# Kernel tuning notes

Hardware: AMD Instinct MI355X
Metric: run time of the kernel (lower is better)

## Reference

```python
import jax, jax.numpy as jnp
import numpy as np

B, N, H = 64, 512, 512
HC = H // 2  # per-direction GRU hidden


def setup_inputs() -> dict:
    key = jax.random.key(0)
    ks = jax.random.split(key, 10)
    s = 0.05
    return {
        "x": jax.random.normal(ks[0], (B, N, H), jnp.float32),
        "num_nodes": jax.random.randint(ks[1], (B,), 1, N + 1),
        "w_ih": jax.random.normal(ks[2], (2, 2, 3 * HC, H), jnp.float32) * s,
        "w_hh": jax.random.normal(ks[3], (2, 2, 3 * HC, HC), jnp.float32) * s,
        "b_ih": jax.random.normal(ks[4], (2, 2, 3 * HC), jnp.float32) * s,
        "b_hh": jax.random.normal(ks[5], (2, 2, 3 * HC), jnp.float32) * s,
        "ln_gamma": jnp.ones((H,), jnp.float32),
        "ln_beta": jnp.zeros((H,), jnp.float32),
        "w_att": jax.random.normal(ks[6], (2 * H, 1), jnp.float32) * s,
        "attention_query": jax.random.normal(ks[7], (B, H), jnp.float32),
    }


def _gru_dir(x, Wih, Whh, bih, bhh, reverse):
    # x: [B, N, in] -> [B, N, HC]; single-direction GRU via lax.scan
    xg = jnp.einsum('bni,gi->bng', x, Wih) + bih  # precompute input gates [B,N,3HC]
    xs = jnp.swapaxes(xg, 0, 1)  # [N, B, 3HC]

    def step(h, xt):
        hg = jnp.einsum('bh,gh->bg', h, Whh) + bhh
        xr, xz, xn = jnp.split(xt, 3, axis=-1)
        hr, hz, hn = jnp.split(hg, 3, axis=-1)
        r = jax.nn.sigmoid(xr + hr)
        z = jax.nn.sigmoid(xz + hz)
        n = jnp.tanh(xn + r * hn)
        h2 = (1.0 - z) * n + z * h
        return h2, h2

    h0 = jnp.zeros((x.shape[0], HC), x.dtype)
    _, ys = jax.lax.scan(step, h0, xs, reverse=reverse)
    return jnp.swapaxes(ys, 0, 1)  # [B, N, HC]


def _residual_gru(x, w_ih, w_hh, b_ih, b_hh, ln_gamma, ln_beta):
    h = x
    for layer in range(2):
        fwd = _gru_dir(h, w_ih[layer, 0], w_hh[layer, 0], b_ih[layer, 0], b_hh[layer, 0], False)
        bwd = _gru_dir(h, w_ih[layer, 1], w_hh[layer, 1], b_ih[layer, 1], b_hh[layer, 1], True)
        h = jnp.concatenate([fwd, bwd], axis=-1)  # [B, N, H]
    y = h + x  # residual
    mu = jnp.mean(y, axis=-1, keepdims=True)
    var = jnp.mean((y - mu) ** 2, axis=-1, keepdims=True)
    return (y - mu) / jnp.sqrt(var + 1e-5) * ln_gamma + ln_beta


def reference(x, num_nodes, w_ih, w_hh, b_ih, b_hh, ln_gamma, ln_beta, w_att, attention_query):
    # zero-pad past each graph's node count (mirrors the torch pad-to-batch loop)
    mask = (jnp.arange(N)[None, :] < num_nodes[:, None])[:, :, None]
    xp = jnp.where(mask, x, 0.0)
    h = _residual_gru(xp, w_ih, w_hh, b_ih, b_hh, ln_gamma, ln_beta)  # [B, N, H]
    # concat([h, query]) @ w_att == h @ w_att[:H] + q @ w_att[H:]
    scores = jnp.einsum('bnh,ho->bno', h, w_att[:H]) + jnp.einsum('bh,ho->bo', attention_query, w_att[H:])[:, None, :]
    scores = jax.nn.leaky_relu(scores, negative_slope=0.01)
    w = jax.nn.softmax(scores, axis=1)  # [B, N, 1] (unmasked, as original)
    return jnp.sum(h * w, axis=1)  # [B, H]
```

## Files before the change

kernel.cpp:

```cpp
#include <hip/hip_runtime.h>
#include <stdint.h>

typedef __attribute__((ext_vector_type(8))) short short8;
typedef __attribute__((ext_vector_type(4))) float f32x4;

#define DEV static __device__ __forceinline__

#define L2E 1.4426950408889634f

DEV unsigned short f2bf(float f){
  unsigned int u = __float_as_uint(f);
  u = (u + 0x7FFFu + ((u >> 16) & 1u)) >> 16;
  return (unsigned short)u;
}
DEV float bf2f(unsigned short u){
  return __uint_as_float(((unsigned int)u) << 16);
}
DEV float frcp(float x){ return __builtin_amdgcn_rcpf(x); }
DEV float exp2a(float x){ float r; asm("v_exp_f32 %0, %1" : "=v"(r) : "v"(x)); return r; }
DEV float bfu(unsigned int u, int c){
  return c ? __uint_as_float(u & 0xFFFF0000u) : __uint_as_float(u << 16);
}
DEV float wredsum(float v){
  #pragma unroll
  for (int m = 32; m; m >>= 1) v += __shfl_xor(v, m);
  return v;
}
DEV float wredmax(float v){
  #pragma unroll
  for (int m = 32; m; m >>= 1) v = fmaxf(v, __shfl_xor(v, m));
  return v;
}

#define BB 64
#define NN 512
#define HH 512
#define HC 256

__global__ void prep_w(const float* __restrict__ wih, const float* __restrict__ whh,
                       const float* __restrict__ bih, const float* __restrict__ bhh,
                       unsigned short* __restrict__ wihb, unsigned short* __restrict__ whhb,
                       float* __restrict__ cbias)
{
  const int NW1 = 2*2*768*512;
  const int NW2 = 2*2*768*256;
  const int NCB = 2*1536;
  for (int i = blockIdx.x*256 + threadIdx.x; i < NW1+NW2+NCB; i += gridDim.x*256){
    if (i < NW1){
      const int row = (i >> 9) % 768;
      const float sc = ((row >> 8) == 2) ? 2.f*L2E : L2E;
      wihb[i] = f2bf(wih[i] * sc);
    } else if (i < NW1+NW2){
      const int k = i - NW1;
      const int row = (k >> 8) % 768;
      const float sc = ((row >> 8) == 2) ? 2.f*L2E : L2E;
      whhb[k] = f2bf(whh[k] * sc);
    } else {
      int k = i - NW1 - NW2;
      int L = k / 1536, r = k % 1536;
      int dd = r / 768, g = r % 768;
      int idx = (L*2 + dd)*768 + g;
      const float sc = (g >= 512) ? 2.f*L2E : L2E;
      cbias[k] = (bih[idx] + (g < 512 ? bhh[idx] : 0.f)) * sc;
    }
  }
}

__global__ void prep_x(const float* __restrict__ x, const int* __restrict__ nnode,
                       unsigned short* __restrict__ xpb)
{
  const int TOT4 = (BB*NN*HH) >> 2;
  for (int i = blockIdx.x*256 + threadIdx.x; i < TOT4; i += gridDim.x*256){
    const int e = i << 2;
    const int b = e >> 18;
    const int n = (e >> 9) & 511;
    float4 v = *(const float4*)(x + e);
    if (n >= nnode[b]) { v.x = 0.f; v.y = 0.f; v.z = 0.f; v.w = 0.f; }
    ushort4 o;
    o.x = f2bf(v.x); o.y = f2bf(v.y); o.z = f2bf(v.z); o.w = f2bf(v.w);
    *(ushort4*)(xpb + e) = o;
  }
}

__global__ __launch_bounds__(256, 2) void gemm_xg(
    const unsigned short* __restrict__ A,
    const unsigned short* __restrict__ W,
    const float* __restrict__ cbias,
    unsigned short* __restrict__ C)
{
  const int tid = threadIdx.x;
  const int l = tid & 63, wv = tid >> 6;
  const int col = l & 15, lq = l >> 4;
  const int n0 = blockIdx.x * 128;
  const int m0 = blockIdx.y * 128;
  const int wm = wv >> 1, wn = wv & 1;
  __shared__ char As[16384];
  __shared__ char Ws[16384];

  f32x4 acc[4][4];
  #pragma unroll
  for (int a = 0; a < 4; a++)
    #pragma unroll
    for (int b2 = 0; b2 < 4; b2++) acc[a][b2] = (f32x4){0.f,0.f,0.f,0.f};

  short8 pa[4], pw[4];
  #pragma unroll
  for (int p = 0; p < 4; p++){
    const int qq = p*256 + tid, row = qq >> 3, sl = qq & 7;
    pa[p] = *(const short8*)(A + (m0+row)*512 + sl*8);
    pw[p] = *(const short8*)(W + (n0+row)*512 + sl*8);
  }

  for (int ko = 0; ko < 8; ++ko){
    __syncthreads();
    #pragma unroll
    for (int p = 0; p < 4; p++){
      const int qq = p*256 + tid, row = qq >> 3, sl = qq & 7;
      *(short8*)(As + row*128 + ((sl ^ (row & 7)) << 4)) = pa[p];
      *(short8*)(Ws + row*128 + ((sl ^ (row & 7)) << 4)) = pw[p];
    }
    __syncthreads();
    if (ko < 7){
      #pragma unroll
      for (int p = 0; p < 4; p++){
        const int qq = p*256 + tid, row = qq >> 3, sl = qq & 7;
        pa[p] = *(const short8*)(A + (m0+row)*512 + (ko+1)*64 + sl*8);
        pw[p] = *(const short8*)(W + (n0+row)*512 + (ko+1)*64 + sl*8);
      }
    }
    #pragma unroll
    for (int kt = 0; kt < 2; kt++){
      short8 af[4], bfr[4];
      #pragma unroll
      for (int mi = 0; mi < 4; mi++){
        const int r = wm*64 + mi*16 + col;
        af[mi] = *(const short8*)(As + r*128 + ((((kt<<2)|lq) ^ (r & 7)) << 4));
      }
      #pragma unroll
      for (int ni = 0; ni < 4; ni++){
        const int r = wn*64 + ni*16 + col;
        bfr[ni] = *(const short8*)(Ws + r*128 + ((((kt<<2)|lq) ^ (r & 7)) << 4));
      }
      #pragma unroll
      for (int mi = 0; mi < 4; mi++)
        #pragma unroll
        for (int ni = 0; ni < 4; ni++)
          acc[mi][ni] = __builtin_amdgcn_mfma_f32_16x16x32_bf16(af[mi], bfr[ni], acc[mi][ni], 0, 0, 0);
    }
  }
  #pragma unroll
  for (int ni = 0; ni < 4; ni++){
    const int n = n0 + wn*64 + ni*16 + col;
    const int dirn = (n >= 768) ? 1 : 0;
    const int g = n - dirn*768;
    const int cls = g >> 8;
    const int j = g & 255;
    const int noff = dirn*768 + (j >> 5)*96 + (j & 15)*6 + cls*2 + ((j >> 4) & 1);
    const float cb = cbias[n];
    #pragma unroll
    for (int mi = 0; mi < 4; mi++){
      const int m = m0 + wm*64 + mi*16 + lq*4;
      #pragma unroll
      for (int rg = 0; rg < 4; rg++)
        C[(m + rg)*1536 + noff] = f2bf(acc[mi][ni][rg] + cb);
    }
  }
}

#define MFMA16(a,b,c) __builtin_amdgcn_mfma_f32_16x16x32_bf16(a, b, c, 0, 0, 0)

#define GRU_STEP(HB_R, HB_W, PF_CUR, PF_NXT, TCUR, TNEXT) do {                  \
  { const uint3 v3 = *(const uint3*)(xg + xgo + (TNEXT)*1536);                  \
    PF_NXT[0]=v3.x; PF_NXT[1]=v3.y; PF_NXT[2]=v3.z; }                           \
  f32x4 acc0 = (f32x4){0.f,0.f,0.f,0.f};                                        \
  f32x4 acc1 = (f32x4){0.f,0.f,0.f,0.f};                                        \
  f32x4 acc2 = (f32x4){0.f,0.f,0.f,0.f};                                        \
  _Pragma("unroll")                                                             \
  for (int kt = 0; kt < 8; kt++){                                               \
    const short8 a = *(const short8*)((HB_R) + kt*64 + lq*16);                  \
    acc0 = MFMA16(a, bw[0][kt], acc0);                                          \
    acc1 = MFMA16(a, bw[1][kt], acc1);                                          \
    const short8 w3 = *(const short8*)(wlds + w*8192 + kt*1024 + l*16);         \
    acc2 = MFMA16(a, w3, acc2);                                                 \
  }                                                                             \
  if (lq == 0){                                                                 \
    const float xr = bfu(PF_CUR[0], hi);                                        \
    const float xz = bfu(PF_CUR[1], hi);                                        \
    const float xn = bfu(PF_CUR[2], hi);                                        \
    const float r_ = frcp(1.f + exp2a(-(xr + acc0[0])));                        \
    const float z_ = frcp(1.f + exp2a(-(xz + acc1[0])));                        \
    const float tt = xn + r_*(acc2[0] + bhn);                                   \
    const float n_ = 1.f - 2.f*frcp(1.f + exp2a(tt));                           \
    const float hn2 = n_ + z_*(hreg - n_);                                      \
    hreg = hn2;                                                                 \
    const unsigned short hb = f2bf(hn2);                                        \
    outb[obo + (TCUR)*512] = hb;                                                \
    *(unsigned short*)((HB_W) + j*2) = hb;                                      \
  }                                                                             \
  __syncthreads();                                                              \
} while(0)

__global__ __launch_bounds__(1024, 4) void gru_rec(
    const unsigned short* __restrict__ xg,
    const unsigned short* __restrict__ whhL,
    const float* __restrict__ bhhL,
    unsigned short* __restrict__ outb)
{
  const int tid = threadIdx.x;
  const int l = tid & 63, w = tid >> 6;
  const int col = l & 15, lq = l >> 4;
  const int dir = blockIdx.x >> 6, bg = blockIdx.x & 63;

  __shared__ char hbuf0[512];
  __shared__ char hbuf1[512];
  __shared__ char wlds[16*8192];

  const unsigned short* whh_d = whhL + dir*768*256;

  short8 bw[2][8];
  #pragma unroll
  for (int i = 0; i < 3; i++){
    const int nt = (i == 0) ? w : (i == 1) ? (16 + w) : (32 + w);
    const int g = nt*16 + col;
    #pragma unroll
    for (int kt = 0; kt < 8; kt++){
      short8 v = *(const short8*)(whh_d + g*256 + kt*32 + lq*8);
      if (i < 2) bw[i][kt] = v;
      else *(short8*)(wlds + w*8192 + kt*1024 + l*16) = v;
    }
  }

  const int j = 16*w + col;
  const float bhn = bhhL[dir*768 + 512 + j] * (2.f*L2E);
  const int hi = w & 1;

  if (tid < 128){
    ((unsigned int*)hbuf0)[tid] = 0u;
    ((unsigned int*)hbuf1)[tid] = 0u;
  }

  float hreg = 0.f;
  const int xgo = bg*(512*1536) + dir*768 + ((w >> 1)*16 + col)*6;
  const int obo = bg*(512*512) + dir*256 + j;

  unsigned int pfA[3], pfB[3];
  const int t0 = dir ? 511 : 0;
  const int dstep = dir ? -1 : 1;
  { const uint3 v3 = *(const uint3*)(xg + xgo + t0*1536);
    pfA[0] = v3.x; pfA[1] = v3.y; pfA[2] = v3.z; }

  __syncthreads();

  int tc = t0;
  #pragma unroll 1
  for (int ss = 0; ss < 256; ss++){
    const int tA = tc;
    const int tB = tA + dstep;
    const int tC = (ss == 255) ? tB : (tB + dstep);
    GRU_STEP(hbuf0, hbuf1, pfA, pfB, tA, tB);
    GRU_STEP(hbuf1, hbuf0, pfB, pfA, tB, tC);
    tc = tC;
  }
}

__global__ void ln_score(
    const unsigned short* __restrict__ h2b, const float* __restrict__ x,
    const int* __restrict__ nnode,
    const float* __restrict__ gam, const float* __restrict__ bet,
    const float* __restrict__ watt,
    float* __restrict__ hln, float* __restrict__ scores)
{
  const int bidx = blockIdx.x;
  const int b = bidx >> 9, n = bidx & 511;
  const int l = threadIdx.x;
  const int base = bidx*512;
  const int i0 = l*8;
  const bool valid = n < nnode[b];

  const short8 hv = *(const short8*)(h2b + base + i0);
  float y[8];
  #pragma unroll
  for (int p = 0; p < 2; p++){
    float4 xv = (float4){0.f,0.f,0.f,0.f};
    if (valid) xv = *(const float4*)(x + base + i0 + p*4);
    y[p*4+0] = bf2f((unsigned short)hv[p*4+0]) + xv.x;
    y[p*4+1] = bf2f((unsigned short)hv[p*4+1]) + xv.y;
    y[p*4+2] = bf2f((unsigned short)hv[p*4+2]) + xv.z;
    y[p*4+3] = bf2f((unsigned short)hv[p*4+3]) + xv.w;
  }
  float s = 0.f, sq = 0.f;
  #pragma unroll
  for (int i = 0; i < 8; i++){ s += y[i]; sq += y[i]*y[i]; }
  s = wredsum(s); sq = wredsum(sq);
  const float mu = s * (1.f/512.f);
  const float rstd = rsqrtf(sq * (1.f/512.f) - mu*mu + 1e-5f);

  float dot = 0.f;
  #pragma unroll
  for (int p = 0; p < 2; p++){
    const float4 gv = *(const float4*)(gam + i0 + p*4);
    const float4 bv = *(const float4*)(bet + i0 + p*4);
    const float4 wv = *(const float4*)(watt + i0 + p*4);
    float4 o;
    o.x = (y[p*4+0] - mu)*rstd*gv.x + bv.x;
    o.y = (y[p*4+1] - mu)*rstd*gv.y + bv.y;
    o.z = (y[p*4+2] - mu)*rstd*gv.z + bv.z;
    o.w = (y[p*4+3] - mu)*rstd*gv.w + bv.w;
    dot += o.x*wv.x + o.y*wv.y + o.z*wv.z + o.w*wv.w;
    *(float4*)(hln + base + i0 + p*4) = o;
  }
  dot = wredsum(dot);
  if (l == 0) scores[bidx] = dot;
}

__global__ void attn_pool(
    const float* __restrict__ hln, const float* __restrict__ scores,
    const float* __restrict__ watt, const float* __restrict__ q,
    float* __restrict__ out)
{
  __shared__ float sc[512];
  __shared__ float red[12];
  const int tid = threadIdx.x, l = tid & 63, w = tid >> 6;
  const int b = blockIdx.x;

  float p = q[b*512 + tid]*watt[512 + tid] + q[b*512 + 256 + tid]*watt[768 + tid];
  p = wredsum(p);
  if (l == 0) red[w] = p;
  __syncthreads();
  const float qd = red[0] + red[1] + red[2] + red[3];

  float s0 = scores[b*512 + tid] + qd;        s0 = s0 > 0.f ? s0 : 0.01f*s0;
  float s1 = scores[b*512 + 256 + tid] + qd;  s1 = s1 > 0.f ? s1 : 0.01f*s1;
  float m_ = wredmax(fmaxf(s0, s1));
  if (l == 0) red[4 + w] = m_;
  __syncthreads();
  const float mx = fmaxf(fmaxf(red[4], red[5]), fmaxf(red[6], red[7]));
  const float e0 = __expf(s0 - mx), e1 = __expf(s1 - mx);
  sc[tid] = e0; sc[tid + 256] = e1;
  float ss = wredsum(e0 + e1);
  if (l == 0) red[8 + w] = ss;
  __syncthreads();
  const float rden = 1.f / (red[8] + red[9] + red[10] + red[11]);

  const int h0 = tid*2;
  float a0 = 0.f, a1 = 0.f;
  for (int t = 0; t < 512; t++){
    const float wv = sc[t];
    const float2 v = *(const float2*)(hln + (b*512 + t)*512 + h0);
    a0 += v.x*wv; a1 += v.y*wv;
  }
  out[b*512 + h0]     = a0 * rden;
  out[b*512 + h0 + 1] = a1 * rden;
}

extern "C" void kernel_launch(void* const* d_in, const int* in_sizes, int n_in,
                              void* d_out, int out_size, void* d_ws, size_t ws_size,
                              hipStream_t stream)
{
  (void)in_sizes; (void)n_in; (void)out_size; (void)ws_size;
  const float* x    = (const float*)d_in[0];
  const int*   nn   = (const int*)d_in[1];
  const float* wih  = (const float*)d_in[2];
  const float* whh  = (const float*)d_in[3];
  const float* bih  = (const float*)d_in[4];
  const float* bhh  = (const float*)d_in[5];
  const float* lg   = (const float*)d_in[6];
  const float* lb   = (const float*)d_in[7];
  const float* watt = (const float*)d_in[8];
  const float* q    = (const float*)d_in[9];
  float* out = (float*)d_out;

  char* ws = (char*)d_ws;
  unsigned short* xg_b = (unsigned short*)(ws + 0);
  unsigned short* xp_b = (unsigned short*)(ws + 100663296);
  unsigned short* h1_b = (unsigned short*)(ws + 134217728);
  unsigned short* h2_b = (unsigned short*)(ws + 167772160);
  unsigned short* wihb = (unsigned short*)(ws + 201326592);
  unsigned short* whhb = (unsigned short*)(ws + 204472320);
  float*         cbias = (float*)(ws + 206045184);
  float*        scores = (float*)(ws + 206057472);
  float*           hln = (float*)(ws + 0);

  prep_w<<<dim3(1024), dim3(256), 0, stream>>>(wih, whh, bih, bhh, wihb, whhb, cbias);
  prep_x<<<dim3(2048), dim3(256), 0, stream>>>(x, nn, xp_b);

  gemm_xg<<<dim3(12, 256), dim3(256), 0, stream>>>(xp_b, wihb, cbias, xg_b);
  gru_rec<<<dim3(128), dim3(1024), 0, stream>>>(xg_b, whhb, bhh, h1_b);

  gemm_xg<<<dim3(12, 256), dim3(256), 0, stream>>>(h1_b, wihb + 1536*512, cbias + 1536, xg_b);
  gru_rec<<<dim3(128), dim3(1024), 0, stream>>>(xg_b, whhb + 2*768*256, bhh + 1536, h2_b);

  ln_score<<<dim3(64*512), dim3(64), 0, stream>>>(h2_b, x, nn, lg, lb, watt, hln, scores);
  attn_pool<<<dim3(64), dim3(256), 0, stream>>>(hln, scores, watt, q, out);
}
```

Measured before the change: 1.354 ms.

## Replace MFMA recurrence with register-resident fp16 dot2 matvec in GRU kernel

The recurrent GRU step no longer runs 16x16x32 bf16 MFMAs, which waste three quarters of the rows on a batch of one. Each thread now keeps 48 uint4 of fp16 W_hh in registers and computes six gate partial dot products with v_dot2 over a quarter of K, then reduces across four lanes with shuffles. The block shrinks to 512 threads, each thread handles two hidden units, and the LDS weight copy is removed. Hidden state is stored as fp16 in a padded LDS buffer. This trades fp16 range and precision for bf16, raises register pressure to roughly 200 VGPRs, and adds shuffle reductions on the serial critical path.

```diff
diff --git a/kernel.cpp b/kernel.cpp
--- a/kernel.cpp
+++ b/kernel.cpp
@@ -3,6 +3,7 @@
 
 typedef __attribute__((ext_vector_type(8))) short short8;
 typedef __attribute__((ext_vector_type(4))) float f32x4;
+typedef __attribute__((ext_vector_type(2))) __fp16 half2v;
 
 #define DEV static __device__ __forceinline__
 
@@ -16,10 +17,15 @@
 DEV float bf2f(unsigned short u){
   return __uint_as_float(((unsigned int)u) << 16);
 }
+DEV unsigned short f2h(float x){
+  const __fp16 h = (__fp16)x;
+  return __builtin_bit_cast(unsigned short, h);
+}
 DEV float frcp(float x){ return __builtin_amdgcn_rcpf(x); }
 DEV float exp2a(float x){ float r; asm("v_exp_f32 %0, %1" : "=v"(r) : "v"(x)); return r; }
-DEV float bfu(unsigned int u, int c){
-  return c ? __uint_as_float(u & 0xFFFF0000u) : __uint_as_float(u << 16);
+DEV float fdot2(unsigned int a, unsigned int b, float c){
+  return __builtin_amdgcn_fdot2(__builtin_bit_cast(half2v, a),
+                                __builtin_bit_cast(half2v, b), c, false);
 }
 DEV float wredsum(float v){
   #pragma unroll
@@ -54,7 +60,7 @@
       const int k = i - NW1;
       const int row = (k >> 8) % 768;
       const float sc = ((row >> 8) == 2) ? 2.f*L2E : L2E;
-      whhb[k] = f2bf(whh[k] * sc);
+      whhb[k] = f2h(whh[k] * sc);
     } else {
       int k = i - NW1 - NW2;
       int L = k / 1536, r = k % 1536;
@@ -167,87 +173,104 @@
   }
 }
 
-#define MFMA16(a,b,c) __builtin_amdgcn_mfma_f32_16x16x32_bf16(a, b, c, 0, 0, 0)
+#define DOT_ROW(HB_R, RR)                                                       \
+  { const uint4 h4 = *(const uint4*)((HB_R) + q*144 + (RR)*16);                 \
+    a0 = fdot2(h4.x, wr[(RR)].x, a0);    a0 = fdot2(h4.y, wr[(RR)].y, a0);      \
+    a0 = fdot2(h4.z, wr[(RR)].z, a0);    a0 = fdot2(h4.w, wr[(RR)].w, a0);      \
+    a1 = fdot2(h4.x, wr[8+(RR)].x, a1);  a1 = fdot2(h4.y, wr[8+(RR)].y, a1);    \
+    a1 = fdot2(h4.z, wr[8+(RR)].z, a1);  a1 = fdot2(h4.w, wr[8+(RR)].w, a1);    \
+    a2 = fdot2(h4.x, wr[16+(RR)].x, a2); a2 = fdot2(h4.y, wr[16+(RR)].y, a2);   \
+    a2 = fdot2(h4.z, wr[16+(RR)].z, a2); a2 = fdot2(h4.w, wr[16+(RR)].w, a2);   \
+    a3 = fdot2(h4.x, wr[24+(RR)].x, a3); a3 = fdot2(h4.y, wr[24+(RR)].y, a3);   \
+    a3 = fdot2(h4.z, wr[24+(RR)].z, a3); a3 = fdot2(h4.w, wr[24+(RR)].w, a3);   \
+    a4 = fdot2(h4.x, wr[32+(RR)].x, a4); a4 = fdot2(h4.y, wr[32+(RR)].y, a4);   \
+    a4 = fdot2(h4.z, wr[32+(RR)].z, a4); a4 = fdot2(h4.w, wr[32+(RR)].w, a4);   \
+    a5 = fdot2(h4.x, wr[40+(RR)].x, a5); a5 = fdot2(h4.y, wr[40+(RR)].y, a5);   \
+    a5 = fdot2(h4.z, wr[40+(RR)].z, a5); a5 = fdot2(h4.w, wr[40+(RR)].w, a5); }
 
 #define GRU_STEP(HB_R, HB_W, PF_CUR, PF_NXT, TCUR, TNEXT) do {                  \
-  { const uint3 v3 = *(const uint3*)(xg + xgo + (TNEXT)*1536);                  \
-    PF_NXT[0]=v3.x; PF_NXT[1]=v3.y; PF_NXT[2]=v3.z; }                           \
-  f32x4 acc0 = (f32x4){0.f,0.f,0.f,0.f};                                        \
-  f32x4 acc1 = (f32x4){0.f,0.f,0.f,0.f};                                        \
-  f32x4 acc2 = (f32x4){0.f,0.f,0.f,0.f};                                        \
   _Pragma("unroll")                                                             \
-  for (int kt = 0; kt < 8; kt++){                                               \
-    const short8 a = *(const short8*)((HB_R) + kt*64 + lq*16);                  \
-    acc0 = MFMA16(a, bw[0][kt], acc0);                                          \
-    acc1 = MFMA16(a, bw[1][kt], acc1);                                          \
-    const short8 w3 = *(const short8*)(wlds + w*8192 + kt*1024 + l*16);         \
-    acc2 = MFMA16(a, w3, acc2);                                                 \
-  }                                                                             \
-  if (lq == 0){                                                                 \
-    const float xr = bfu(PF_CUR[0], hi);                                        \
-    const float xz = bfu(PF_CUR[1], hi);                                        \
-    const float xn = bfu(PF_CUR[2], hi);                                        \
-    const float r_ = frcp(1.f + exp2a(-(xr + acc0[0])));                        \
-    const float z_ = frcp(1.f + exp2a(-(xz + acc1[0])));                        \
-    const float tt = xn + r_*(acc2[0] + bhn);                                   \
-    const float n_ = 1.f - 2.f*frcp(1.f + exp2a(tt));                           \
-    const float hn2 = n_ + z_*(hreg - n_);                                      \
-    hreg = hn2;                                                                 \
-    const unsigned short hb = f2bf(hn2);                                        \
-    outb[obo + (TCUR)*512] = hb;                                                \
-    *(unsigned short*)((HB_W) + j*2) = hb;                                      \
+  for (int i6 = 0; i6 < 6; i6++)                                                \
+    PF_NXT[i6] = xg[xbase + (TNEXT)*1536 + xo[i6]];                             \
+  float a0=0.f, a1=0.f, a2=0.f, a3=0.f, a4=0.f, a5=0.f;                         \
+  DOT_ROW(HB_R, 0) DOT_ROW(HB_R, 1) DOT_ROW(HB_R, 2) DOT_ROW(HB_R, 3)          \
+  DOT_ROW(HB_R, 4) DOT_ROW(HB_R, 5) DOT_ROW(HB_R, 6) DOT_ROW(HB_R, 7)          \
+  a0 += __shfl_xor(a0, 1); a0 += __shfl_xor(a0, 2);                             \
+  a1 += __shfl_xor(a1, 1); a1 += __shfl_xor(a1, 2);                             \
+  a2 += __shfl_xor(a2, 1); a2 += __shfl_xor(a2, 2);                             \
+  a3 += __shfl_xor(a3, 1); a3 += __shfl_xor(a3, 2);                             \
+  a4 += __shfl_xor(a4, 1); a4 += __shfl_xor(a4, 2);                             \
+  a5 += __shfl_xor(a5, 1); a5 += __shfl_xor(a5, 2);                             \
+  const float r0 = frcp(1.f + exp2a(-(bf2f(PF_CUR[0]) + a0)));                  \
+  const float r1 = frcp(1.f + exp2a(-(bf2f(PF_CUR[1]) + a1)));                  \
+  const float z0 = frcp(1.f + exp2a(-(bf2f(PF_CUR[2]) + a2)));                  \
+  const float z1 = frcp(1.f + exp2a(-(bf2f(PF_CUR[3]) + a3)));                  \
+  const float tt0 = bf2f(PF_CUR[4]) + r0*(a4 + bhn0);                           \
+  const float tt1 = bf2f(PF_CUR[5]) + r1*(a5 + bhn1);                           \
+  const float n0 = 1.f - 2.f*frcp(1.f + exp2a(tt0));                            \
+  const float n1 = 1.f - 2.f*frcp(1.f + exp2a(tt1));                            \
+  const float h0 = n0 + z0*(hr0 - n0);                                          \
+  const float h1 = n1 + z1*(hr1 - n1);                                          \
+  hr0 = h0; hr1 = h1;                                                           \
+  if (q == 0){                                                                  \
+    ((unsigned int*)outb)[obo + (TCUR)*256] =                                   \
+        (unsigned int)f2bf(h0) | ((unsigned int)f2bf(h1) << 16);                \
+    *(unsigned int*)((HB_W) + hwo) =                                            \
+        (unsigned int)f2h(h0) | ((unsigned int)f2h(h1) << 16);                  \
   }                                                                             \
   __syncthreads();                                                              \
 } while(0)
 
-__global__ __launch_bounds__(1024, 4) void gru_rec(
+__global__ __launch_bounds__(512, 2) void gru_rec(
     const unsigned short* __restrict__ xg,
-    const unsigned short* __restrict__ whhL,
+    const unsigned short* __restrict__ whhF,
     const float* __restrict__ bhhL,
     unsigned short* __restrict__ outb)
 {
   const int tid = threadIdx.x;
   const int l = tid & 63, w = tid >> 6;
-  const int col = l & 15, lq = l >> 4;
+  const int q = l & 3, p = l >> 2;
   const int dir = blockIdx.x >> 6, bg = blockIdx.x & 63;
 
-  __shared__ char hbuf0[512];
-  __shared__ char hbuf1[512];
-  __shared__ char wlds[16*8192];
-
-  const unsigned short* whh_d = whhL + dir*768*256;
-
-  short8 bw[2][8];
-  #pragma unroll
-  for (int i = 0; i < 3; i++){
-    const int nt = (i == 0) ? w : (i == 1) ? (16 + w) : (32 + w);
-    const int g = nt*16 + col;
+  __shared__ char hb[1152];
+  char* const hb0 = hb;
+  char* const hb1 = hb + 576;
+
+  const unsigned short* whh_d = whhF + dir*768*256;
+  const int j0 = w*32 + 2*p, j1 = j0 + 1;
+
+  uint4 wr[48];
+  #pragma unroll
+  for (int gi = 0; gi < 6; gi++){
+    const int g = (gi >> 1)*256 + ((gi & 1) ? j1 : j0);
     #pragma unroll
-    for (int kt = 0; kt < 8; kt++){
-      short8 v = *(const short8*)(whh_d + g*256 + kt*32 + lq*8);
-      if (i < 2) bw[i][kt] = v;
-      else *(short8*)(wlds + w*8192 + kt*1024 + l*16) = v;
-    }
-  }
-
-  const int j = 16*w + col;
-  const float bhn = bhhL[dir*768 + 512 + j] * (2.f*L2E);
-  const int hi = w & 1;
-
-  if (tid < 128){
-    ((unsigned int*)hbuf0)[tid] = 0u;
-    ((unsigned int*)hbuf1)[tid] = 0u;
-  }
-
-  float hreg = 0.f;
-  const int xgo = bg*(512*1536) + dir*768 + ((w >> 1)*16 + col)*6;
-  const int obo = bg*(512*512) + dir*256 + j;
-
-  unsigned int pfA[3], pfB[3];
+    for (int r = 0; r < 8; r++)
+      wr[gi*8 + r] = *(const uint4*)(whh_d + g*256 + q*64 + r*8);
+  }
+
+  const float bhn0 = bhhL[dir*768 + 512 + j0] * (2.f*L2E);
+  const float bhn1 = bhhL[dir*768 + 512 + j1] * (2.f*L2E);
+
+  for (int z = tid; z < 288; z += 512) ((unsigned int*)hb)[z] = 0u;
+
+  float hr0 = 0.f, hr1 = 0.f;
+
+  int xo[6];
+  #pragma unroll
+  for (int gi = 0; gi < 6; gi++){
+    const int jj = (gi & 1) ? j1 : j0;
+    const int cls = gi >> 1;
+    xo[gi] = (jj >> 5)*96 + (jj & 15)*6 + cls*2 + ((jj >> 4) & 1);
+  }
+  const int xbase = bg*(512*1536) + dir*768;
+  const int obo = (bg*(512*512) + dir*256 + j0) >> 1;
+  const int hwo = (j0 >> 6)*144 + (j0 & 63)*2;
+
+  unsigned short pfA[6], pfB[6];
   const int t0 = dir ? 511 : 0;
   const int dstep = dir ? -1 : 1;
-  { const uint3 v3 = *(const uint3*)(xg + xgo + t0*1536);
-    pfA[0] = v3.x; pfA[1] = v3.y; pfA[2] = v3.z; }
+  #pragma unroll
+  for (int i6 = 0; i6 < 6; i6++) pfA[i6] = xg[xbase + t0*1536 + xo[i6]];
 
   __syncthreads();
 
@@ -257,8 +280,8 @@
     const int tA = tc;
     const int tB = tA + dstep;
     const int tC = (ss == 255) ? tB : (tB + dstep);
-    GRU_STEP(hbuf0, hbuf1, pfA, pfB, tA, tB);
-    GRU_STEP(hbuf1, hbuf0, pfB, pfA, tB, tC);
+    GRU_STEP(hb0, hb1, pfA, pfB, tA, tB);
+    GRU_STEP(hb1, hb0, pfB, pfA, tB, tC);
     tc = tC;
   }
 }
@@ -385,10 +408,10 @@
   prep_x<<<dim3(2048), dim3(256), 0, stream>>>(x, nn, xp_b);
 
   gemm_xg<<<dim3(12, 256), dim3(256), 0, stream>>>(xp_b, wihb, cbias, xg_b);
-  gru_rec<<<dim3(128), dim3(1024), 0, stream>>>(xg_b, whhb, bhh, h1_b);
+  gru_rec<<<dim3(128), dim3(512), 0, stream>>>(xg_b, whhb, bhh, h1_b);
 
   gemm_xg<<<dim3(12, 256), dim3(256), 0, stream>>>(h1_b, wihb + 1536*512, cbias + 1536, xg_b);
-  gru_rec<<<dim3(128), dim3(1024), 0, stream>>>(xg_b, whhb + 2*768*256, bhh + 1536, h2_b);
+  gru_rec<<<dim3(128), dim3(512), 0, stream>>>(xg_b, whhb + 2*768*256, bhh + 1536, h2_b);
 
   ln_score<<<dim3(64*512), dim3(64), 0, stream>>>(h2_b, x, nn, lg, lb, watt, hln, scores);
   attn_pool<<<dim3(64), dim3(256), 0, stream>>>(hln, scores, watt, q, out);
```

After: 1.650 ms. +21.9%, slower.
